# Kernel optimization log

Hardware: AMD Instinct MI355X
Metric: run time of the kernel (lower is better)

Reference implementation:

```python
import jax, jax.numpy as jnp
import numpy as np

B, T, D = 2, 1024, 768
H, HS = 12, 64          # n_head, head_size = n_embed // n_head
E, K = 8, 1             # num_experts, top-k (MoeLayer default k=1)
DF = 4 * D              # FFN hidden
EPS = 1e-5


def _ln(x, g, b):
    mu = jnp.mean(x, axis=-1, keepdims=True)
    var = jnp.mean(jnp.square(x - mu), axis=-1, keepdims=True)
    return (x - mu) * jax.lax.rsqrt(var + EPS) * g + b


def setup_inputs() -> dict:
    key = jax.random.key(0)
    ks = jax.random.split(key, 12)
    s = 0.02
    return {
        "x": jax.random.normal(ks[0], (B, T, D), dtype=jnp.float32),
        "ln1_g": jnp.ones((D,), jnp.float32),
        "ln1_b": jnp.zeros((D,), jnp.float32),
        "ln2_g": jnp.ones((D,), jnp.float32),
        "ln2_b": jnp.zeros((D,), jnp.float32),
        "Wq": jax.random.normal(ks[1], (H, D, HS), jnp.float32) * s,
        "Wk": jax.random.normal(ks[2], (H, D, HS), jnp.float32) * s,
        "Wv": jax.random.normal(ks[3], (H, D, HS), jnp.float32) * s,
        "Wp": jax.random.normal(ks[4], (D, D), jnp.float32) * s,
        "bp": jnp.zeros((D,), jnp.float32),
        "Wg": jax.random.normal(ks[5], (D, E), jnp.float32) * s,
        "W1": jax.random.normal(ks[6], (E, D, DF), jnp.float32) * s,
        "b1": jnp.zeros((E, DF), jnp.float32),
        "W2": jax.random.normal(ks[7], (E, DF, D), jnp.float32) * s,
        "b2": jnp.zeros((E, D), jnp.float32),
    }


def reference(x, ln1_g, ln1_b, ln2_g, ln2_b, Wq, Wk, Wv, Wp, bp, Wg, W1, b1, W2, b2):
    b, t, d = x.shape

    # ---- multi-head causal self-attention (per-head QKV, as in Head) ----
    h = _ln(x, ln1_g, ln1_b)
    q = jnp.einsum('btd,hds->bhts', h, Wq)
    k = jnp.einsum('btd,hds->bhts', h, Wk)
    v = jnp.einsum('btd,hds->bhts', h, Wv)
    # NOTE: original scales by C**-0.5 with C = n_embed (not head_size)
    scores = jnp.einsum('bhts,bhus->bhtu', q, k) * (d ** -0.5)
    causal = jnp.tril(jnp.ones((t, t), dtype=bool))
    scores = jnp.where(causal, scores, -jnp.inf)
    att = jax.nn.softmax(scores, axis=-1)
    out = jnp.einsum('bhtu,bhus->bhts', att, v)          # [B,H,T,HS]
    out = out.transpose(0, 2, 1, 3).reshape(b, t, d)     # concat heads
    x = x + out @ Wp + bp

    # ---- top-k MoE feed-forward (MoeLayer, k=1) ----
    h2 = _ln(x, ln2_g, ln2_b).reshape(-1, d)             # [N,D]
    gate_logits = h2 @ Wg                                # [N,E]
    w, sel = jax.lax.top_k(gate_logits, K)               # [N,K]
    w = jax.nn.softmax(w.astype(jnp.float32), axis=-1).astype(x.dtype)
    n = h2.shape[0]
    combine = jnp.zeros((n, Wg.shape[1]), x.dtype).at[
        jnp.arange(n)[:, None], sel].add(w)              # [N,E]
    hid = jax.nn.relu(jnp.einsum('nd,edf->enf', h2, W1) + b1[:, None, :])
    y = jnp.einsum('enf,efd->end', hid, W2) + b2[:, None, :]
    moe = jnp.einsum('ne,end->nd', combine, y)           # dense dispatch
    return x + moe.reshape(b, t, d)
```

## Files before the change

kernel.cpp:

```cpp
#include <hip/hip_runtime.h>
#include <math.h>

typedef __bf16 bf16;
typedef __bf16 bf16x8 __attribute__((ext_vector_type(8)));
typedef float f32x4 __attribute__((ext_vector_type(4)));

#define N_TOK 2048
#define DMODEL 768
#define NHEAD 12
#define TSEQ 1024
#define NEXP 8
#define DFF 3072

__device__ inline f32x4 mfma16(bf16x8 a, bf16x8 b, f32x4 c) {
    return __builtin_amdgcn_mfma_f32_16x16x32_bf16(a, b, c, 0, 0, 0);
}

__device__ inline f32x4 zero4() { f32x4 z = {0.f, 0.f, 0.f, 0.f}; return z; }

__device__ inline float block_sum(float v, float* red, int tid) {
#pragma unroll
    for (int off = 32; off > 0; off >>= 1) v += __shfl_down(v, off, 64);
    __syncthreads();
    if ((tid & 63) == 0) red[tid >> 6] = v;
    __syncthreads();
    return red[0] + red[1] + red[2] + red[3];
}

__global__ __launch_bounds__(256) void ln1_kernel(const float* __restrict__ x,
        const float* __restrict__ g, const float* __restrict__ b,
        bf16* __restrict__ hh, bf16* __restrict__ hl) {
    __shared__ float red[4];
    int row = blockIdx.x, tid = threadIdx.x;
    const float* xr = x + (size_t)row * DMODEL;
    float v[3];
#pragma unroll
    for (int i = 0; i < 3; i++) v[i] = xr[tid + i * 256];
    float s = block_sum(v[0] + v[1] + v[2], red, tid);
    float mu = s * (1.f / DMODEL);
    float q = 0.f;
#pragma unroll
    for (int i = 0; i < 3; i++) { float d = v[i] - mu; q += d * d; }
    q = block_sum(q, red, tid);
    float rstd = 1.0f / sqrtf(q * (1.f / DMODEL) + 1e-5f);
#pragma unroll
    for (int i = 0; i < 3; i++) {
        int d = tid + i * 256;
        float val = (v[i] - mu) * rstd * g[d] + b[d];
        bf16 hi = (bf16)val;
        hh[(size_t)row * DMODEL + d] = hi;
        hl[(size_t)row * DMODEL + d] = (bf16)(val - (float)hi);
    }
}

__device__ inline void gemm_step3(const bf16* lah, const bf16* lal,
                                  const bf16* lbh, const bf16* lbl,
                                  int wm, int wn, int row16, int quad,
                                  f32x4 acc[4][4]) {
    bf16x8 ah[4], al[4], bh[4], bl[4];
#pragma unroll
    for (int i = 0; i < 4; i++) {
        int ro = (wm * 64 + i * 16 + row16) * 40 + quad * 8;
        ah[i] = *(const bf16x8*)&lah[ro];
        al[i] = *(const bf16x8*)&lal[ro];
    }
#pragma unroll
    for (int i = 0; i < 4; i++) {
        int ro = (wn * 64 + i * 16 + row16) * 40 + quad * 8;
        bh[i] = *(const bf16x8*)&lbh[ro];
        bl[i] = *(const bf16x8*)&lbl[ro];
    }
#pragma unroll
    for (int mi = 0; mi < 4; mi++)
#pragma unroll
        for (int ni = 0; ni < 4; ni++) {
            acc[mi][ni] = mfma16(ah[mi], bh[ni], acc[mi][ni]);
            acc[mi][ni] = mfma16(ah[mi], bl[ni], acc[mi][ni]);
            acc[mi][ni] = mfma16(al[mi], bh[ni], acc[mi][ni]);
        }
}

__device__ inline void gemm_step1(const bf16* la, const bf16* lb, int wm, int wn,
                                  int row16, int quad, f32x4 acc[4][4]) {
    bf16x8 af[4], bfr[4];
#pragma unroll
    for (int i = 0; i < 4; i++)
        af[i] = *(const bf16x8*)&la[(wm * 64 + i * 16 + row16) * 40 + quad * 8];
#pragma unroll
    for (int i = 0; i < 4; i++)
        bfr[i] = *(const bf16x8*)&lb[(wn * 64 + i * 16 + row16) * 40 + quad * 8];
#pragma unroll
    for (int mi = 0; mi < 4; mi++)
#pragma unroll
        for (int ni = 0; ni < 4; ni++)
            acc[mi][ni] = mfma16(af[mi], bfr[ni], acc[mi][ni]);
}

#define TILE_E (128 * 40)

__global__ __launch_bounds__(256) void qkv_gemm(const bf16* __restrict__ hA_h,
        const bf16* __restrict__ hA_l,
        const float* __restrict__ Wq, const float* __restrict__ Wk,
        const float* __restrict__ Wv,
        bf16* __restrict__ qh, bf16* __restrict__ ql,
        bf16* __restrict__ kh, bf16* __restrict__ kl,
        bf16* __restrict__ vh, bf16* __restrict__ vl) {
    __shared__ alignas(16) bf16 lah[2 * TILE_E];
    __shared__ alignas(16) bf16 lal[2 * TILE_E];
    __shared__ alignas(16) bf16 lbh[2 * TILE_E];
    __shared__ alignas(16) bf16 lbl[2 * TILE_E];
    int tid = threadIdx.x;
    int m0 = blockIdx.y * 128;
    int nt = blockIdx.x;
    int sel = nt / 6;
    int n0 = (nt % 6) * 128;
    const float* W = (sel == 0) ? Wq : (sel == 1) ? Wk : Wv;
    bf16* obh = (sel == 0) ? qh : (sel == 1) ? kh : vh;
    bf16* obl = (sel == 0) ? ql : (sel == 1) ? kl : vl;
    int lane = tid & 63, w = tid >> 6, row16 = lane & 15, quad = lane >> 4;
    int wm = w >> 1, wn = w & 1;
    int r_a = tid >> 2, c_a = (tid & 3) << 3;
    int nW = tid & 127, kbase = tid >> 7;
    size_t wcol = (size_t)((n0 + nW) >> 6) * DMODEL * 64 + ((n0 + nW) & 63);
    f32x4 acc[4][4];
#pragma unroll
    for (int mi = 0; mi < 4; mi++)
#pragma unroll
        for (int ni = 0; ni < 4; ni++) acc[mi][ni] = zero4();
    const bf16* Ah = hA_h + (size_t)m0 * DMODEL;
    const bf16* Al = hA_l + (size_t)m0 * DMODEL;

    bf16x8 rAh0, rAh1, rAl0, rAl1;
    float wv[16];
    rAh0 = *(const bf16x8*)&Ah[(size_t)r_a * DMODEL + c_a];
    rAh1 = *(const bf16x8*)&Ah[(size_t)(r_a + 64) * DMODEL + c_a];
    rAl0 = *(const bf16x8*)&Al[(size_t)r_a * DMODEL + c_a];
    rAl1 = *(const bf16x8*)&Al[(size_t)(r_a + 64) * DMODEL + c_a];
#pragma unroll
    for (int i = 0; i < 16; i++) wv[i] = W[wcol + (size_t)(kbase + 2 * i) * 64];
    *(bf16x8*)&lah[r_a * 40 + c_a] = rAh0;
    *(bf16x8*)&lah[(r_a + 64) * 40 + c_a] = rAh1;
    *(bf16x8*)&lal[r_a * 40 + c_a] = rAl0;
    *(bf16x8*)&lal[(r_a + 64) * 40 + c_a] = rAl1;
#pragma unroll
    for (int i = 0; i < 16; i++) {
        bf16 hi = (bf16)wv[i];
        lbh[nW * 40 + kbase + 2 * i] = hi;
        lbl[nW * 40 + kbase + 2 * i] = (bf16)(wv[i] - (float)hi);
    }
    const int nk = DMODEL / 32;
    for (int ki = 0; ki < nk; ki++) {
        __syncthreads();
        int cur = (ki & 1) * TILE_E, nxt = ((ki + 1) & 1) * TILE_E;
        if (ki + 1 < nk) {
            int k0 = (ki + 1) * 32;
            rAh0 = *(const bf16x8*)&Ah[(size_t)r_a * DMODEL + k0 + c_a];
            rAh1 = *(const bf16x8*)&Ah[(size_t)(r_a + 64) * DMODEL + k0 + c_a];
            rAl0 = *(const bf16x8*)&Al[(size_t)r_a * DMODEL + k0 + c_a];
            rAl1 = *(const bf16x8*)&Al[(size_t)(r_a + 64) * DMODEL + k0 + c_a];
#pragma unroll
            for (int i = 0; i < 16; i++)
                wv[i] = W[wcol + (size_t)(k0 + kbase + 2 * i) * 64];
        }
        gemm_step3(lah + cur, lal + cur, lbh + cur, lbl + cur, wm, wn, row16, quad, acc);
        if (ki + 1 < nk) {
            *(bf16x8*)&lah[nxt + r_a * 40 + c_a] = rAh0;
            *(bf16x8*)&lah[nxt + (r_a + 64) * 40 + c_a] = rAh1;
            *(bf16x8*)&lal[nxt + r_a * 40 + c_a] = rAl0;
            *(bf16x8*)&lal[nxt + (r_a + 64) * 40 + c_a] = rAl1;
#pragma unroll
            for (int i = 0; i < 16; i++) {
                bf16 hi = (bf16)wv[i];
                lbh[nxt + nW * 40 + kbase + 2 * i] = hi;
                lbl[nxt + nW * 40 + kbase + 2 * i] = (bf16)(wv[i] - (float)hi);
            }
        }
    }
#pragma unroll
    for (int mi = 0; mi < 4; mi++) {
        int rowl = wm * 64 + mi * 16 + quad * 4;
#pragma unroll
        for (int ni = 0; ni < 4; ni++) {
            int col = n0 + wn * 64 + ni * 16 + row16;
            int hhd = col >> 6, s = col & 63;
#pragma unroll
            for (int r = 0; r < 4; r++) {
                int gm = m0 + rowl + r;
                int bb = gm >> 10, t = gm & 1023;
                size_t oi = (((size_t)bb * NHEAD + hhd) * TSEQ + t) * 64 + s;
                float val = acc[mi][ni][r];
                bf16 hi = (bf16)val;
                obh[oi] = hi;
                obl[oi] = (bf16)(val - (float)hi);
            }
        }
    }
}

__global__ __launch_bounds__(256) void attn_kernel(const bf16* __restrict__ qhb,
        const bf16* __restrict__ qlb, const bf16* __restrict__ khb,
        const bf16* __restrict__ klb, const bf16* __restrict__ vhb,
        const bf16* __restrict__ vlb, bf16* __restrict__ aoh,
        bf16* __restrict__ aol) {
    __shared__ alignas(16) bf16 kt_h[64 * 72];
    __shared__ alignas(16) bf16 kt_l[64 * 72];
    __shared__ alignas(16) bf16 vt_h[64 * 72];
    __shared__ alignas(16) bf16 vt_l[64 * 72];
    __shared__ alignas(16) bf16 p_h[4][16 * 72];
    __shared__ alignas(16) bf16 p_l[4][16 * 72];
    int qt = blockIdx.x, bh = blockIdx.y;
    int b = bh / NHEAD, hh = bh % NHEAD;
    int tid = threadIdx.x, lane = tid & 63, w = tid >> 6;
    int row16 = lane & 15, quad = lane >> 4;
    const bf16* qph = qhb + (size_t)bh * TSEQ * 64;
    const bf16* qpl = qlb + (size_t)bh * TSEQ * 64;
    const bf16* kph = khb + (size_t)bh * TSEQ * 64;
    const bf16* kpl = klb + (size_t)bh * TSEQ * 64;
    const bf16* vph = vhb + (size_t)bh * TSEQ * 64;
    const bf16* vpl = vlb + (size_t)bh * TSEQ * 64;
    int qrow = qt * 64 + w * 16 + row16;
    bf16x8 aq_h[2], aq_l[2];
#pragma unroll
    for (int kk = 0; kk < 2; kk++) {
        aq_h[kk] = *(const bf16x8*)&qph[(size_t)qrow * 64 + kk * 32 + quad * 8];
        aq_l[kk] = *(const bf16x8*)&qpl[(size_t)qrow * 64 + kk * 32 + quad * 8];
    }
    f32x4 o[4];
    float m_i[4], l_i[4];
#pragma unroll
    for (int i = 0; i < 4; i++) { o[i] = zero4(); m_i[i] = -INFINITY; l_i[i] = 0.f; }
    const float sc = 0.03608439182435161f;
    for (int kt = 0; kt <= qt; kt++) {
        __syncthreads();
#pragma unroll
        for (int i = 0; i < 2; i++) {
            int chunk = tid + i * 256;
            int r = chunk >> 3, c = (chunk & 7) << 3;
            size_t gi = (size_t)(kt * 64 + r) * 64 + c;
            *(bf16x8*)&kt_h[r * 72 + c] = *(const bf16x8*)&kph[gi];
            *(bf16x8*)&kt_l[r * 72 + c] = *(const bf16x8*)&kpl[gi];
        }
#pragma unroll
        for (int i = 0; i < 16; i++) {
            int idx = tid + (i << 8);
            int tk = idx >> 6, s = idx & 63;
            size_t gi = (size_t)(kt * 64 + tk) * 64 + s;
            vt_h[s * 72 + tk] = vph[gi];
            vt_l[s * 72 + tk] = vpl[gi];
        }
        __syncthreads();
        f32x4 sacc[4];
#pragma unroll
        for (int ni = 0; ni < 4; ni++) {
            sacc[ni] = zero4();
#pragma unroll
            for (int kk = 0; kk < 2; kk++) {
                int ro = (ni * 16 + row16) * 72 + kk * 32 + quad * 8;
                bf16x8 bk_h = *(const bf16x8*)&kt_h[ro];
                bf16x8 bk_l = *(const bf16x8*)&kt_l[ro];
                sacc[ni] = mfma16(aq_h[kk], bk_h, sacc[ni]);
                sacc[ni] = mfma16(aq_h[kk], bk_l, sacc[ni]);
                sacc[ni] = mfma16(aq_l[kk], bk_h, sacc[ni]);
            }
        }
        float mrow[4];
#pragma unroll
        for (int r = 0; r < 4; r++) mrow[r] = -INFINITY;
        int tq_b = qt * 64 + w * 16 + quad * 4;
#pragma unroll
        for (int ni = 0; ni < 4; ni++) {
            int tkg = kt * 64 + ni * 16 + row16;
#pragma unroll
            for (int r = 0; r < 4; r++) {
                float sv = sacc[ni][r] * sc;
                if (tkg > tq_b + r) sv = -INFINITY;
                sacc[ni][r] = sv;
                mrow[r] = fmaxf(mrow[r], sv);
            }
        }
#pragma unroll
        for (int r = 0; r < 4; r++) {
#pragma unroll
            for (int off = 8; off > 0; off >>= 1)
                mrow[r] = fmaxf(mrow[r], __shfl_xor(mrow[r], off, 16));
        }
        float alpha[4], rsum[4];
#pragma unroll
        for (int r = 0; r < 4; r++) {
            float nm = fmaxf(m_i[r], mrow[r]);
            alpha[r] = __expf(m_i[r] - nm);
            m_i[r] = nm;
            rsum[r] = 0.f;
        }
#pragma unroll
        for (int ni = 0; ni < 4; ni++)
#pragma unroll
            for (int r = 0; r < 4; r++) {
                float p = __expf(sacc[ni][r] - m_i[r]);
                sacc[ni][r] = p;
                rsum[r] += p;
            }
#pragma unroll
        for (int r = 0; r < 4; r++) {
#pragma unroll
            for (int off = 8; off > 0; off >>= 1)
                rsum[r] += __shfl_xor(rsum[r], off, 16);
            l_i[r] = l_i[r] * alpha[r] + rsum[r];
        }
#pragma unroll
        for (int ni = 0; ni < 4; ni++)
#pragma unroll
            for (int r = 0; r < 4; r++) o[ni][r] *= alpha[r];
#pragma unroll
        for (int ni = 0; ni < 4; ni++)
#pragma unroll
            for (int r = 0; r < 4; r++) {
                float p = sacc[ni][r];
                bf16 hi = (bf16)p;
                int po = (quad * 4 + r) * 72 + ni * 16 + row16;
                p_h[w][po] = hi;
                p_l[w][po] = (bf16)(p - (float)hi);
            }
        __syncthreads();
        bf16x8 ap_h[2], ap_l[2];
#pragma unroll
        for (int kk = 0; kk < 2; kk++) {
            ap_h[kk] = *(const bf16x8*)&p_h[w][row16 * 72 + kk * 32 + quad * 8];
            ap_l[kk] = *(const bf16x8*)&p_l[w][row16 * 72 + kk * 32 + quad * 8];
        }
#pragma unroll
        for (int ni = 0; ni < 4; ni++)
#pragma unroll
            for (int kk = 0; kk < 2; kk++) {
                int ro = (ni * 16 + row16) * 72 + kk * 32 + quad * 8;
                bf16x8 bv_h = *(const bf16x8*)&vt_h[ro];
                bf16x8 bv_l = *(const bf16x8*)&vt_l[ro];
                o[ni] = mfma16(ap_h[kk], bv_h, o[ni]);
                o[ni] = mfma16(ap_h[kk], bv_l, o[ni]);
                o[ni] = mfma16(ap_l[kk], bv_h, o[ni]);
            }
    }
    int t = qt * 64 + w * 16 + quad * 4;
#pragma unroll
    for (int ni = 0; ni < 4; ni++) {
        int col = hh * 64 + ni * 16 + row16;
#pragma unroll
        for (int r = 0; r < 4; r++) {
            float val = o[ni][r] / l_i[r];
            size_t n = (size_t)b * TSEQ + t + r;
            bf16 hi = (bf16)val;
            aoh[n * DMODEL + col] = hi;
            aol[n * DMODEL + col] = (bf16)(val - (float)hi);
        }
    }
}

__global__ __launch_bounds__(256) void proj_gemm(const bf16* __restrict__ aInH,
        const bf16* __restrict__ aInL,
        const float* __restrict__ Wp, const float* __restrict__ bp,
        const float* __restrict__ x, float* __restrict__ x1) {
    __shared__ alignas(16) bf16 lah[2 * TILE_E];
    __shared__ alignas(16) bf16 lal[2 * TILE_E];
    __shared__ alignas(16) bf16 lbh[2 * TILE_E];
    __shared__ alignas(16) bf16 lbl[2 * TILE_E];
    int tid = threadIdx.x;
    int m0 = blockIdx.y * 128, n0 = blockIdx.x * 128;
    int lane = tid & 63, w = tid >> 6, row16 = lane & 15, quad = lane >> 4;
    int wm = w >> 1, wn = w & 1;
    int r_a = tid >> 2, c_a = (tid & 3) << 3;
    int nW = tid & 127, kbase = tid >> 7;
    f32x4 acc[4][4];
#pragma unroll
    for (int mi = 0; mi < 4; mi++)
#pragma unroll
        for (int ni = 0; ni < 4; ni++) acc[mi][ni] = zero4();
    const bf16* Ah = aInH + (size_t)m0 * DMODEL;
    const bf16* Al = aInL + (size_t)m0 * DMODEL;
    bf16x8 rAh0, rAh1, rAl0, rAl1;
    float wv[16];
    rAh0 = *(const bf16x8*)&Ah[(size_t)r_a * DMODEL + c_a];
    rAh1 = *(const bf16x8*)&Ah[(size_t)(r_a + 64) * DMODEL + c_a];
    rAl0 = *(const bf16x8*)&Al[(size_t)r_a * DMODEL + c_a];
    rAl1 = *(const bf16x8*)&Al[(size_t)(r_a + 64) * DMODEL + c_a];
#pragma unroll
    for (int i = 0; i < 16; i++)
        wv[i] = Wp[(size_t)(kbase + 2 * i) * DMODEL + n0 + nW];
    *(bf16x8*)&lah[r_a * 40 + c_a] = rAh0;
    *(bf16x8*)&lah[(r_a + 64) * 40 + c_a] = rAh1;
    *(bf16x8*)&lal[r_a * 40 + c_a] = rAl0;
    *(bf16x8*)&lal[(r_a + 64) * 40 + c_a] = rAl1;
#pragma unroll
    for (int i = 0; i < 16; i++) {
        bf16 hi = (bf16)wv[i];
        lbh[nW * 40 + kbase + 2 * i] = hi;
        lbl[nW * 40 + kbase + 2 * i] = (bf16)(wv[i] - (float)hi);
    }
    const int nk = DMODEL / 32;
    for (int ki = 0; ki < nk; ki++) {
        __syncthreads();
        int cur = (ki & 1) * TILE_E, nxt = ((ki + 1) & 1) * TILE_E;
        if (ki + 1 < nk) {
            int k0 = (ki + 1) * 32;
            rAh0 = *(const bf16x8*)&Ah[(size_t)r_a * DMODEL + k0 + c_a];
            rAh1 = *(const bf16x8*)&Ah[(size_t)(r_a + 64) * DMODEL + k0 + c_a];
            rAl0 = *(const bf16x8*)&Al[(size_t)r_a * DMODEL + k0 + c_a];
            rAl1 = *(const bf16x8*)&Al[(size_t)(r_a + 64) * DMODEL + k0 + c_a];
#pragma unroll
            for (int i = 0; i < 16; i++)
                wv[i] = Wp[(size_t)(k0 + kbase + 2 * i) * DMODEL + n0 + nW];
        }
        gemm_step3(lah + cur, lal + cur, lbh + cur, lbl + cur, wm, wn, row16, quad, acc);
        if (ki + 1 < nk) {
            *(bf16x8*)&lah[nxt + r_a * 40 + c_a] = rAh0;
            *(bf16x8*)&lah[nxt + (r_a + 64) * 40 + c_a] = rAh1;
            *(bf16x8*)&lal[nxt + r_a * 40 + c_a] = rAl0;
            *(bf16x8*)&lal[nxt + (r_a + 64) * 40 + c_a] = rAl1;
#pragma unroll
            for (int i = 0; i < 16; i++) {
                bf16 hi = (bf16)wv[i];
                lbh[nxt + nW * 40 + kbase + 2 * i] = hi;
                lbl[nxt + nW * 40 + kbase + 2 * i] = (bf16)(wv[i] - (float)hi);
            }
        }
    }
#pragma unroll
    for (int mi = 0; mi < 4; mi++) {
        int rowl = wm * 64 + mi * 16 + quad * 4;
#pragma unroll
        for (int ni = 0; ni < 4; ni++) {
            int col = n0 + wn * 64 + ni * 16 + row16;
#pragma unroll
            for (int r = 0; r < 4; r++) {
                int gm = m0 + rowl + r;
                x1[(size_t)gm * DMODEL + col] =
                    acc[mi][ni][r] + bp[col] + x[(size_t)gm * DMODEL + col];
            }
        }
    }
}

__global__ __launch_bounds__(256) void ln2_gate_kernel(const float* __restrict__ x1,
        const float* __restrict__ g, const float* __restrict__ b,
        const float* __restrict__ Wg, bf16* __restrict__ h2,
        int* __restrict__ sel, int* __restrict__ counts) {
    __shared__ float red[4];
    __shared__ float glog[8];
    int row = blockIdx.x, tid = threadIdx.x;
    if (tid < 8) glog[tid] = 0.f;
    const float* xr = x1 + (size_t)row * DMODEL;
    float v[3];
#pragma unroll
    for (int i = 0; i < 3; i++) v[i] = xr[tid + i * 256];
    float s = block_sum(v[0] + v[1] + v[2], red, tid);
    float mu = s * (1.f / DMODEL);
    float qv = 0.f;
#pragma unroll
    for (int i = 0; i < 3; i++) { float d = v[i] - mu; qv += d * d; }
    qv = block_sum(qv, red, tid);
    float rstd = 1.0f / sqrtf(qv * (1.f / DMODEL) + 1e-5f);
    float ga[8];
#pragma unroll
    for (int e = 0; e < 8; e++) ga[e] = 0.f;
#pragma unroll
    for (int i = 0; i < 3; i++) {
        int d = tid + i * 256;
        float hv = (v[i] - mu) * rstd * g[d] + b[d];
        h2[(size_t)row * DMODEL + d] = (bf16)hv;
        const float* wgr = Wg + (size_t)d * NEXP;
#pragma unroll
        for (int e = 0; e < 8; e++) ga[e] += hv * wgr[e];
    }
#pragma unroll
    for (int e = 0; e < 8; e++)
#pragma unroll
        for (int off = 32; off > 0; off >>= 1) ga[e] += __shfl_down(ga[e], off, 64);
    if ((tid & 63) == 0)
#pragma unroll
        for (int e = 0; e < 8; e++) atomicAdd(&glog[e], ga[e]);
    __syncthreads();
    if (tid == 0) {
        float best = glog[0];
        int bi = 0;
#pragma unroll
        for (int e = 1; e < 8; e++)
            if (glog[e] > best) { best = glog[e]; bi = e; }
        sel[row] = bi;
        atomicAdd(&counts[bi], 1);
    }
}

__global__ void zero_kernel(int* __restrict__ p, int n) {
    int i = blockIdx.x * blockDim.x + threadIdx.x;
    if (i < n) p[i] = 0;
}
__global__ void zero_out_kernel(float* __restrict__ p) {
    int i = blockIdx.x * blockDim.x + threadIdx.x;
    f32x4 z = zero4();
    *(f32x4*)&p[i * 4] = z;
}
__global__ void scan_kernel(const int* __restrict__ counts, int* __restrict__ offsets) {
    if (threadIdx.x == 0) {
        int o = 0;
        for (int e = 0; e < NEXP; e++) { offsets[e] = o; o += counts[e]; }
    }
}
__global__ void scatter_kernel(const int* __restrict__ sel, const int* __restrict__ offsets,
                               int* __restrict__ cursor, int* __restrict__ perm) {
    int n = blockIdx.x * blockDim.x + threadIdx.x;
    if (n >= N_TOK) return;
    int e = sel[n];
    int pos = atomicAdd(&cursor[e], 1);
    perm[offsets[e] + pos] = n;
}

__global__ __launch_bounds__(256) void moe1_gemm(const bf16* __restrict__ h2,
        const float* __restrict__ W1, const float* __restrict__ b1,
        const int* __restrict__ counts, const int* __restrict__ offsets,
        const int* __restrict__ perm, bf16* __restrict__ hid) {
    int e = blockIdx.z;
    int cnt = counts[e];
    int rt = blockIdx.y;
    if (rt * 128 >= cnt) return;
    int off = offsets[e];
    int n0 = blockIdx.x * 128;
    const float* W = W1 + (size_t)e * DMODEL * DFF;
    __shared__ alignas(16) bf16 la[2 * TILE_E];
    __shared__ alignas(16) bf16 lb[2 * TILE_E];
    int tid = threadIdx.x;
    int lane = tid & 63, w = tid >> 6, row16 = lane & 15, quad = lane >> 4;
    int wm = w >> 1, wn = w & 1;
    int r_a = tid >> 2, c_a = (tid & 3) << 3;
    int nW = tid & 127, kbase = tid >> 7;
    int tok0 = perm[off + min(rt * 128 + r_a, cnt - 1)];
    int tok1 = perm[off + min(rt * 128 + r_a + 64, cnt - 1)];
    const bf16* a0 = h2 + (size_t)tok0 * DMODEL;
    const bf16* a1 = h2 + (size_t)tok1 * DMODEL;
    f32x4 acc[4][4];
#pragma unroll
    for (int mi = 0; mi < 4; mi++)
#pragma unroll
        for (int ni = 0; ni < 4; ni++) acc[mi][ni] = zero4();
    bf16x8 rA0, rA1;
    float wv[16];
    rA0 = *(const bf16x8*)&a0[c_a];
    rA1 = *(const bf16x8*)&a1[c_a];
#pragma unroll
    for (int i = 0; i < 16; i++)
        wv[i] = W[(size_t)(kbase + 2 * i) * DFF + n0 + nW];
    *(bf16x8*)&la[r_a * 40 + c_a] = rA0;
    *(bf16x8*)&la[(r_a + 64) * 40 + c_a] = rA1;
#pragma unroll
    for (int i = 0; i < 16; i++) lb[nW * 40 + kbase + 2 * i] = (bf16)wv[i];
    const int nk = DMODEL / 32;
    for (int ki = 0; ki < nk; ki++) {
        __syncthreads();
        int cur = (ki & 1) * TILE_E, nxt = ((ki + 1) & 1) * TILE_E;
        if (ki + 1 < nk) {
            int k0 = (ki + 1) * 32;
            rA0 = *(const bf16x8*)&a0[k0 + c_a];
            rA1 = *(const bf16x8*)&a1[k0 + c_a];
#pragma unroll
            for (int i = 0; i < 16; i++)
                wv[i] = W[(size_t)(k0 + kbase + 2 * i) * DFF + n0 + nW];
        }
        gemm_step1(la + cur, lb + cur, wm, wn, row16, quad, acc);
        if (ki + 1 < nk) {
            *(bf16x8*)&la[nxt + r_a * 40 + c_a] = rA0;
            *(bf16x8*)&la[nxt + (r_a + 64) * 40 + c_a] = rA1;
#pragma unroll
            for (int i = 0; i < 16; i++) lb[nxt + nW * 40 + kbase + 2 * i] = (bf16)wv[i];
        }
    }
#pragma unroll
    for (int mi = 0; mi < 4; mi++) {
        int rowl = wm * 64 + mi * 16 + quad * 4;
#pragma unroll
        for (int ni = 0; ni < 4; ni++) {
            int col = n0 + wn * 64 + ni * 16 + row16;
#pragma unroll
            for (int r = 0; r < 4; r++) {
                int lr = rowl + r;
                if (rt * 128 + lr < cnt) {
                    float val = acc[mi][ni][r] + b1[(size_t)e * DFF + col];
                    val = fmaxf(val, 0.f);
                    hid[(size_t)(off + rt * 128 + lr) * DFF + col] = (bf16)val;
                }
            }
        }
    }
}

__global__ __launch_bounds__(256) void moe2_gemm(const bf16* __restrict__ hid,
        const float* __restrict__ W2, const float* __restrict__ b2,
        const int* __restrict__ counts, const int* __restrict__ offsets,
        const int* __restrict__ perm, const float* __restrict__ x1,
        float* __restrict__ out) {
    int ez = blockIdx.z;
    int e = ez >> 1, ks = ez & 1;
    int cnt = counts[e];
    int rt = blockIdx.y;
    if (rt * 128 >= cnt) return;
    int off = offsets[e];
    int n0 = blockIdx.x * 128;
    const float* W = W2 + (size_t)e * DFF * DMODEL;
    __shared__ alignas(16) bf16 la[2 * TILE_E];
    __shared__ alignas(16) bf16 lb[2 * TILE_E];
    int tid = threadIdx.x;
    int lane = tid & 63, w = tid >> 6, row16 = lane & 15, quad = lane >> 4;
    int wm = w >> 1, wn = w & 1;
    int r_a = tid >> 2, c_a = (tid & 3) << 3;
    int nW = tid & 127, kbase = tid >> 7;
    const bf16* a0 = hid + (size_t)min(off + rt * 128 + r_a, N_TOK - 1) * DFF;
    const bf16* a1 = hid + (size_t)min(off + rt * 128 + r_a + 64, N_TOK - 1) * DFF;
    f32x4 acc[4][4];
#pragma unroll
    for (int mi = 0; mi < 4; mi++)
#pragma unroll
        for (int ni = 0; ni < 4; ni++) acc[mi][ni] = zero4();
    const int kst = ks * (DFF / 2);
    bf16x8 rA0, rA1;
    float wv[16];
    rA0 = *(const bf16x8*)&a0[kst + c_a];
    rA1 = *(const bf16x8*)&a1[kst + c_a];
#pragma unroll
    for (int i = 0; i < 16; i++)
        wv[i] = W[(size_t)(kst + kbase + 2 * i) * DMODEL + n0 + nW];
    *(bf16x8*)&la[r_a * 40 + c_a] = rA0;
    *(bf16x8*)&la[(r_a + 64) * 40 + c_a] = rA1;
#pragma unroll
    for (int i = 0; i < 16; i++) lb[nW * 40 + kbase + 2 * i] = (bf16)wv[i];
    const int nk = (DFF / 2) / 32;
    for (int ki = 0; ki < nk; ki++) {
        __syncthreads();
        int cur = (ki & 1) * TILE_E, nxt = ((ki + 1) & 1) * TILE_E;
        if (ki + 1 < nk) {
            int k0 = kst + (ki + 1) * 32;
            rA0 = *(const bf16x8*)&a0[k0 + c_a];
            rA1 = *(const bf16x8*)&a1[k0 + c_a];
#pragma unroll
            for (int i = 0; i < 16; i++)
                wv[i] = W[(size_t)(k0 + kbase + 2 * i) * DMODEL + n0 + nW];
        }
        gemm_step1(la + cur, lb + cur, wm, wn, row16, quad, acc);
        if (ki + 1 < nk) {
            *(bf16x8*)&la[nxt + r_a * 40 + c_a] = rA0;
            *(bf16x8*)&la[nxt + (r_a + 64) * 40 + c_a] = rA1;
#pragma unroll
            for (int i = 0; i < 16; i++) lb[nxt + nW * 40 + kbase + 2 * i] = (bf16)wv[i];
        }
    }
#pragma unroll
    for (int mi = 0; mi < 4; mi++) {
        int rowl = wm * 64 + mi * 16 + quad * 4;
#pragma unroll
        for (int ni = 0; ni < 4; ni++) {
            int col = n0 + wn * 64 + ni * 16 + row16;
#pragma unroll
            for (int r = 0; r < 4; r++) {
                int lr = rowl + r;
                if (rt * 128 + lr < cnt) {
                    int n = perm[off + rt * 128 + lr];
                    float val = acc[mi][ni][r];
                    if (ks == 0)
                        val += b2[(size_t)e * DMODEL + col] + x1[(size_t)n * DMODEL + col];
                    atomicAdd(&out[(size_t)n * DMODEL + col], val);
                }
            }
        }
    }
}

extern "C" void kernel_launch(void* const* d_in, const int* in_sizes, int n_in,
                              void* d_out, int out_size, void* d_ws, size_t ws_size,
                              hipStream_t stream) {
    const float* x    = (const float*)d_in[0];
    const float* ln1g = (const float*)d_in[1];
    const float* ln1b = (const float*)d_in[2];
    const float* ln2g = (const float*)d_in[3];
    const float* ln2b = (const float*)d_in[4];
    const float* Wq   = (const float*)d_in[5];
    const float* Wk   = (const float*)d_in[6];
    const float* Wv   = (const float*)d_in[7];
    const float* Wp   = (const float*)d_in[8];
    const float* bp   = (const float*)d_in[9];
    const float* Wg   = (const float*)d_in[10];
    const float* W1   = (const float*)d_in[11];
    const float* b1   = (const float*)d_in[12];
    const float* W2   = (const float*)d_in[13];
    const float* b2   = (const float*)d_in[14];
    float* out = (float*)d_out;

    char* ws = (char*)d_ws;
    size_t off = 0;
    const size_t SZ = (size_t)N_TOK * DMODEL * 2;
    bf16* h1h = (bf16*)(ws + off); off += SZ;
    bf16* h1l = (bf16*)(ws + off); off += SZ;
    bf16* qh  = (bf16*)(ws + off); off += SZ;
    bf16* ql  = (bf16*)(ws + off); off += SZ;
    bf16* kh  = (bf16*)(ws + off); off += SZ;
    bf16* kl  = (bf16*)(ws + off); off += SZ;
    bf16* vh  = (bf16*)(ws + off); off += SZ;
    bf16* vl  = (bf16*)(ws + off); off += SZ;
    bf16* aoh = (bf16*)(ws + off); off += SZ;
    bf16* aol = (bf16*)(ws + off); off += SZ;
    float* x1 = (float*)(ws + off); off += (size_t)N_TOK * DMODEL * 4;
    bf16* h2  = (bf16*)(ws + off); off += SZ;
    bf16* hid = (bf16*)(ws + off); off += (size_t)N_TOK * DFF * 2;
    int* counts  = (int*)(ws + off); off += 8 * 4;
    int* cursor  = (int*)(ws + off); off += 8 * 4;
    int* offsets = (int*)(ws + off); off += 8 * 4;
    int* sel     = (int*)(ws + off); off += (size_t)N_TOK * 4;
    int* perm    = (int*)(ws + off); off += (size_t)N_TOK * 4;

    zero_kernel<<<1, 64, 0, stream>>>(counts, 16);
    zero_out_kernel<<<N_TOK * DMODEL / 4 / 256, 256, 0, stream>>>(out);
    ln1_kernel<<<N_TOK, 256, 0, stream>>>(x, ln1g, ln1b, h1h, h1l);
    qkv_gemm<<<dim3(18, 16), 256, 0, stream>>>(h1h, h1l, Wq, Wk, Wv, qh, ql, kh, kl, vh, vl);
    attn_kernel<<<dim3(16, 24), 256, 0, stream>>>(qh, ql, kh, kl, vh, vl, aoh, aol);
    proj_gemm<<<dim3(6, 16), 256, 0, stream>>>(aoh, aol, Wp, bp, x, x1);
    ln2_gate_kernel<<<N_TOK, 256, 0, stream>>>(x1, ln2g, ln2b, Wg, h2, sel, counts);
    scan_kernel<<<1, 64, 0, stream>>>(counts, offsets);
    scatter_kernel<<<8, 256, 0, stream>>>(sel, offsets, cursor, perm);
    moe1_gemm<<<dim3(24, 16, 8), 256, 0, stream>>>(h2, W1, b1, counts, offsets, perm, hid);
    moe2_gemm<<<dim3(6, 16, 16), 256, 0, stream>>>(hid, W2, b2, counts, offsets, perm, x1, out);
}
```

Measured before the change: 540.0 us.

## Fold zeroing and scan into other kernels, vectorize LDS weight stores, widen MoE2 split-K

Drops the zero, zero_out and scan launches. Zeroing of counts and the output moves into ln1_kernel, and each consumer recomputes expert offsets from counts. Weight staging now gives each thread 16 contiguous k values, so the converted bf16 values go to LDS as 4-wide vector stores instead of scalar strided ones. The V transpose in attention also packs 4 values per LDS store. MoE2 split-K goes from 2 to 4 slices to get more blocks, at the cost of more atomicAdds into the output.

```diff
diff --git a/kernel.cpp b/kernel.cpp
--- a/kernel.cpp
+++ b/kernel.cpp
@@ -2,6 +2,7 @@
 #include <math.h>
 
 typedef __bf16 bf16;
+typedef __bf16 bf16x4 __attribute__((ext_vector_type(4)));
 typedef __bf16 bf16x8 __attribute__((ext_vector_type(8)));
 typedef float f32x4 __attribute__((ext_vector_type(4)));
 
@@ -29,9 +30,13 @@
 
 __global__ __launch_bounds__(256) void ln1_kernel(const float* __restrict__ x,
         const float* __restrict__ g, const float* __restrict__ b,
-        bf16* __restrict__ hh, bf16* __restrict__ hl) {
+        bf16* __restrict__ hh, bf16* __restrict__ hl,
+        int* __restrict__ cz, float* __restrict__ outz) {
     __shared__ float red[4];
     int row = blockIdx.x, tid = threadIdx.x;
+    if (row == 0 && tid < 16) cz[tid] = 0;
+#pragma unroll
+    for (int i = 0; i < 3; i++) outz[(size_t)row * DMODEL + tid + i * 256] = 0.f;
     const float* xr = x + (size_t)row * DMODEL;
     float v[3];
 #pragma unroll
@@ -97,6 +102,31 @@
 }
 
 #define TILE_E (128 * 40)
+
+__device__ inline void wstore_hilo(bf16* lbh, bf16* lbl, int base, const float* wv) {
+#pragma unroll
+    for (int gq = 0; gq < 4; gq++) {
+        bf16x4 ph, pl;
+#pragma unroll
+        for (int j = 0; j < 4; j++) {
+            float v = wv[gq * 4 + j];
+            bf16 hi = (bf16)v;
+            ph[j] = hi;
+            pl[j] = (bf16)(v - (float)hi);
+        }
+        *(bf16x4*)&lbh[base + gq * 4] = ph;
+        *(bf16x4*)&lbl[base + gq * 4] = pl;
+    }
+}
+__device__ inline void wstore1(bf16* lb, int base, const float* wv) {
+#pragma unroll
+    for (int gq = 0; gq < 4; gq++) {
+        bf16x4 p;
+#pragma unroll
+        for (int j = 0; j < 4; j++) p[j] = (bf16)wv[gq * 4 + j];
+        *(bf16x4*)&lb[base + gq * 4] = p;
+    }
+}
 
 __global__ __launch_bounds__(256) void qkv_gemm(const bf16* __restrict__ hA_h,
         const bf16* __restrict__ hA_l,
@@ -120,8 +150,9 @@
     int lane = tid & 63, w = tid >> 6, row16 = lane & 15, quad = lane >> 4;
     int wm = w >> 1, wn = w & 1;
     int r_a = tid >> 2, c_a = (tid & 3) << 3;
-    int nW = tid & 127, kbase = tid >> 7;
+    int nW = tid & 127, kb16 = (tid >> 7) * 16;
     size_t wcol = (size_t)((n0 + nW) >> 6) * DMODEL * 64 + ((n0 + nW) & 63);
+    int wbase = nW * 40 + kb16;
     f32x4 acc[4][4];
 #pragma unroll
     for (int mi = 0; mi < 4; mi++)
@@ -129,7 +160,6 @@
         for (int ni = 0; ni < 4; ni++) acc[mi][ni] = zero4();
     const bf16* Ah = hA_h + (size_t)m0 * DMODEL;
     const bf16* Al = hA_l + (size_t)m0 * DMODEL;
-
     bf16x8 rAh0, rAh1, rAl0, rAl1;
     float wv[16];
     rAh0 = *(const bf16x8*)&Ah[(size_t)r_a * DMODEL + c_a];
@@ -137,17 +167,12 @@
     rAl0 = *(const bf16x8*)&Al[(size_t)r_a * DMODEL + c_a];
     rAl1 = *(const bf16x8*)&Al[(size_t)(r_a + 64) * DMODEL + c_a];
 #pragma unroll
-    for (int i = 0; i < 16; i++) wv[i] = W[wcol + (size_t)(kbase + 2 * i) * 64];
+    for (int i = 0; i < 16; i++) wv[i] = W[wcol + (size_t)(kb16 + i) * 64];
     *(bf16x8*)&lah[r_a * 40 + c_a] = rAh0;
     *(bf16x8*)&lah[(r_a + 64) * 40 + c_a] = rAh1;
     *(bf16x8*)&lal[r_a * 40 + c_a] = rAl0;
     *(bf16x8*)&lal[(r_a + 64) * 40 + c_a] = rAl1;
-#pragma unroll
-    for (int i = 0; i < 16; i++) {
-        bf16 hi = (bf16)wv[i];
-        lbh[nW * 40 + kbase + 2 * i] = hi;
-        lbl[nW * 40 + kbase + 2 * i] = (bf16)(wv[i] - (float)hi);
-    }
+    wstore_hilo(lbh, lbl, wbase, wv);
     const int nk = DMODEL / 32;
     for (int ki = 0; ki < nk; ki++) {
         __syncthreads();
@@ -160,7 +185,7 @@
             rAl1 = *(const bf16x8*)&Al[(size_t)(r_a + 64) * DMODEL + k0 + c_a];
 #pragma unroll
             for (int i = 0; i < 16; i++)
-                wv[i] = W[wcol + (size_t)(k0 + kbase + 2 * i) * 64];
+                wv[i] = W[wcol + (size_t)(k0 + kb16 + i) * 64];
         }
         gemm_step3(lah + cur, lal + cur, lbh + cur, lbl + cur, wm, wn, row16, quad, acc);
         if (ki + 1 < nk) {
@@ -168,12 +193,7 @@
             *(bf16x8*)&lah[nxt + (r_a + 64) * 40 + c_a] = rAh1;
             *(bf16x8*)&lal[nxt + r_a * 40 + c_a] = rAl0;
             *(bf16x8*)&lal[nxt + (r_a + 64) * 40 + c_a] = rAl1;
-#pragma unroll
-            for (int i = 0; i < 16; i++) {
-                bf16 hi = (bf16)wv[i];
-                lbh[nxt + nW * 40 + kbase + 2 * i] = hi;
-                lbl[nxt + nW * 40 + kbase + 2 * i] = (bf16)(wv[i] - (float)hi);
-            }
+            wstore_hilo(lbh + nxt, lbl + nxt, wbase, wv);
         }
     }
 #pragma unroll
@@ -241,12 +261,18 @@
             *(bf16x8*)&kt_l[r * 72 + c] = *(const bf16x8*)&kpl[gi];
         }
 #pragma unroll
-        for (int i = 0; i < 16; i++) {
-            int idx = tid + (i << 8);
-            int tk = idx >> 6, s = idx & 63;
-            size_t gi = (size_t)(kt * 64 + tk) * 64 + s;
-            vt_h[s * 72 + tk] = vph[gi];
-            vt_l[s * 72 + tk] = vpl[gi];
+        for (int u = 0; u < 4; u++) {
+            int unit = tid + u * 256;
+            int s = unit & 63, tg = unit >> 6;
+            bf16x4 ph, pl;
+#pragma unroll
+            for (int j = 0; j < 4; j++) {
+                size_t gi = (size_t)(kt * 64 + tg * 4 + j) * 64 + s;
+                ph[j] = vph[gi];
+                pl[j] = vpl[gi];
+            }
+            *(bf16x4*)&vt_h[s * 72 + tg * 4] = ph;
+            *(bf16x4*)&vt_l[s * 72 + tg * 4] = pl;
         }
         __syncthreads();
         f32x4 sacc[4];
@@ -368,7 +394,8 @@
     int lane = tid & 63, w = tid >> 6, row16 = lane & 15, quad = lane >> 4;
     int wm = w >> 1, wn = w & 1;
     int r_a = tid >> 2, c_a = (tid & 3) << 3;
-    int nW = tid & 127, kbase = tid >> 7;
+    int nW = tid & 127, kb16 = (tid >> 7) * 16;
+    int wbase = nW * 40 + kb16;
     f32x4 acc[4][4];
 #pragma unroll
     for (int mi = 0; mi < 4; mi++)
@@ -384,17 +411,12 @@
     rAl1 = *(const bf16x8*)&Al[(size_t)(r_a + 64) * DMODEL + c_a];
 #pragma unroll
     for (int i = 0; i < 16; i++)
-        wv[i] = Wp[(size_t)(kbase + 2 * i) * DMODEL + n0 + nW];
+        wv[i] = Wp[(size_t)(kb16 + i) * DMODEL + n0 + nW];
     *(bf16x8*)&lah[r_a * 40 + c_a] = rAh0;
     *(bf16x8*)&lah[(r_a + 64) * 40 + c_a] = rAh1;
     *(bf16x8*)&lal[r_a * 40 + c_a] = rAl0;
     *(bf16x8*)&lal[(r_a + 64) * 40 + c_a] = rAl1;
-#pragma unroll
-    for (int i = 0; i < 16; i++) {
-        bf16 hi = (bf16)wv[i];
-        lbh[nW * 40 + kbase + 2 * i] = hi;
-        lbl[nW * 40 + kbase + 2 * i] = (bf16)(wv[i] - (float)hi);
-    }
+    wstore_hilo(lbh, lbl, wbase, wv);
     const int nk = DMODEL / 32;
     for (int ki = 0; ki < nk; ki++) {
         __syncthreads();
@@ -407,7 +429,7 @@
             rAl1 = *(const bf16x8*)&Al[(size_t)(r_a + 64) * DMODEL + k0 + c_a];
 #pragma unroll
             for (int i = 0; i < 16; i++)
-                wv[i] = Wp[(size_t)(k0 + kbase + 2 * i) * DMODEL + n0 + nW];
+                wv[i] = Wp[(size_t)(k0 + kb16 + i) * DMODEL + n0 + nW];
         }
         gemm_step3(lah + cur, lal + cur, lbh + cur, lbl + cur, wm, wn, row16, quad, acc);
         if (ki + 1 < nk) {
@@ -415,12 +437,7 @@
             *(bf16x8*)&lah[nxt + (r_a + 64) * 40 + c_a] = rAh1;
             *(bf16x8*)&lal[nxt + r_a * 40 + c_a] = rAl0;
             *(bf16x8*)&lal[nxt + (r_a + 64) * 40 + c_a] = rAl1;
-#pragma unroll
-            for (int i = 0; i < 16; i++) {
-                bf16 hi = (bf16)wv[i];
-                lbh[nxt + nW * 40 + kbase + 2 * i] = hi;
-                lbl[nxt + nW * 40 + kbase + 2 * i] = (bf16)(wv[i] - (float)hi);
-            }
+            wstore_hilo(lbh + nxt, lbl + nxt, wbase, wv);
         }
     }
 #pragma unroll
@@ -489,39 +506,27 @@
     }
 }
 
-__global__ void zero_kernel(int* __restrict__ p, int n) {
-    int i = blockIdx.x * blockDim.x + threadIdx.x;
-    if (i < n) p[i] = 0;
-}
-__global__ void zero_out_kernel(float* __restrict__ p) {
-    int i = blockIdx.x * blockDim.x + threadIdx.x;
-    f32x4 z = zero4();
-    *(f32x4*)&p[i * 4] = z;
-}
-__global__ void scan_kernel(const int* __restrict__ counts, int* __restrict__ offsets) {
-    if (threadIdx.x == 0) {
-        int o = 0;
-        for (int e = 0; e < NEXP; e++) { offsets[e] = o; o += counts[e]; }
-    }
-}
-__global__ void scatter_kernel(const int* __restrict__ sel, const int* __restrict__ offsets,
+__global__ void scatter_kernel(const int* __restrict__ sel, const int* __restrict__ counts,
                                int* __restrict__ cursor, int* __restrict__ perm) {
     int n = blockIdx.x * blockDim.x + threadIdx.x;
     if (n >= N_TOK) return;
     int e = sel[n];
+    int off = 0;
+    for (int i = 0; i < NEXP; i++) off += (i < e) ? counts[i] : 0;
     int pos = atomicAdd(&cursor[e], 1);
-    perm[offsets[e] + pos] = n;
+    perm[off + pos] = n;
 }
 
 __global__ __launch_bounds__(256) void moe1_gemm(const bf16* __restrict__ h2,
         const float* __restrict__ W1, const float* __restrict__ b1,
-        const int* __restrict__ counts, const int* __restrict__ offsets,
-        const int* __restrict__ perm, bf16* __restrict__ hid) {
+        const int* __restrict__ counts, const int* __restrict__ perm,
+        bf16* __restrict__ hid) {
     int e = blockIdx.z;
     int cnt = counts[e];
     int rt = blockIdx.y;
     if (rt * 128 >= cnt) return;
-    int off = offsets[e];
+    int off = 0;
+    for (int i = 0; i < NEXP; i++) off += (i < e) ? counts[i] : 0;
     int n0 = blockIdx.x * 128;
     const float* W = W1 + (size_t)e * DMODEL * DFF;
     __shared__ alignas(16) bf16 la[2 * TILE_E];
@@ -530,7 +535,8 @@
     int lane = tid & 63, w = tid >> 6, row16 = lane & 15, quad = lane >> 4;
     int wm = w >> 1, wn = w & 1;
     int r_a = tid >> 2, c_a = (tid & 3) << 3;
-    int nW = tid & 127, kbase = tid >> 7;
+    int nW = tid & 127, kb16 = (tid >> 7) * 16;
+    int wbase = nW * 40 + kb16;
     int tok0 = perm[off + min(rt * 128 + r_a, cnt - 1)];
     int tok1 = perm[off + min(rt * 128 + r_a + 64, cnt - 1)];
     const bf16* a0 = h2 + (size_t)tok0 * DMODEL;
@@ -546,11 +552,10 @@
     rA1 = *(const bf16x8*)&a1[c_a];
 #pragma unroll
     for (int i = 0; i < 16; i++)
-        wv[i] = W[(size_t)(kbase + 2 * i) * DFF + n0 + nW];
+        wv[i] = W[(size_t)(kb16 + i) * DFF + n0 + nW];
     *(bf16x8*)&la[r_a * 40 + c_a] = rA0;
     *(bf16x8*)&la[(r_a + 64) * 40 + c_a] = rA1;
-#pragma unroll
-    for (int i = 0; i < 16; i++) lb[nW * 40 + kbase + 2 * i] = (bf16)wv[i];
+    wstore1(lb, wbase, wv);
     const int nk = DMODEL / 32;
     for (int ki = 0; ki < nk; ki++) {
         __syncthreads();
@@ -561,14 +566,13 @@
             rA1 = *(const bf16x8*)&a1[k0 + c_a];
 #pragma unroll
             for (int i = 0; i < 16; i++)
-                wv[i] = W[(size_t)(k0 + kbase + 2 * i) * DFF + n0 + nW];
+                wv[i] = W[(size_t)(k0 + kb16 + i) * DFF + n0 + nW];
         }
         gemm_step1(la + cur, lb + cur, wm, wn, row16, quad, acc);
         if (ki + 1 < nk) {
             *(bf16x8*)&la[nxt + r_a * 40 + c_a] = rA0;
             *(bf16x8*)&la[nxt + (r_a + 64) * 40 + c_a] = rA1;
-#pragma unroll
-            for (int i = 0; i < 16; i++) lb[nxt + nW * 40 + kbase + 2 * i] = (bf16)wv[i];
+            wstore1(lb + nxt, wbase, wv);
         }
     }
 #pragma unroll
@@ -592,15 +596,15 @@
 
 __global__ __launch_bounds__(256) void moe2_gemm(const bf16* __restrict__ hid,
         const float* __restrict__ W2, const float* __restrict__ b2,
-        const int* __restrict__ counts, const int* __restrict__ offsets,
-        const int* __restrict__ perm, const float* __restrict__ x1,
-        float* __restrict__ out) {
+        const int* __restrict__ counts, const int* __restrict__ perm,
+        const float* __restrict__ x1, float* __restrict__ out) {
     int ez = blockIdx.z;
-    int e = ez >> 1, ks = ez & 1;
+    int e = ez & 7, ks = ez >> 3;
     int cnt = counts[e];
     int rt = blockIdx.y;
     if (rt * 128 >= cnt) return;
-    int off = offsets[e];
+    int off = 0;
+    for (int i = 0; i < NEXP; i++) off += (i < e) ? counts[i] : 0;
     int n0 = blockIdx.x * 128;
     const float* W = W2 + (size_t)e * DFF * DMODEL;
     __shared__ alignas(16) bf16 la[2 * TILE_E];
@@ -609,7 +613,8 @@
     int lane = tid & 63, w = tid >> 6, row16 = lane & 15, quad = lane >> 4;
     int wm = w >> 1, wn = w & 1;
     int r_a = tid >> 2, c_a = (tid & 3) << 3;
-    int nW = tid & 127, kbase = tid >> 7;
+    int nW = tid & 127, kb16 = (tid >> 7) * 16;
+    int wbase = nW * 40 + kb16;
     const bf16* a0 = hid + (size_t)min(off + rt * 128 + r_a, N_TOK - 1) * DFF;
     const bf16* a1 = hid + (size_t)min(off + rt * 128 + r_a + 64, N_TOK - 1) * DFF;
     f32x4 acc[4][4];
@@ -617,19 +622,18 @@
     for (int mi = 0; mi < 4; mi++)
 #pragma unroll
         for (int ni = 0; ni < 4; ni++) acc[mi][ni] = zero4();
-    const int kst = ks * (DFF / 2);
+    const int kst = ks * (DFF / 4);
     bf16x8 rA0, rA1;
     float wv[16];
     rA0 = *(const bf16x8*)&a0[kst + c_a];
     rA1 = *(const bf16x8*)&a1[kst + c_a];
 #pragma unroll
     for (int i = 0; i < 16; i++)
-        wv[i] = W[(size_t)(kst + kbase + 2 * i) * DMODEL + n0 + nW];
+        wv[i] = W[(size_t)(kst + kb16 + i) * DMODEL + n0 + nW];
     *(bf16x8*)&la[r_a * 40 + c_a] = rA0;
     *(bf16x8*)&la[(r_a + 64) * 40 + c_a] = rA1;
-#pragma unroll
-    for (int i = 0; i < 16; i++) lb[nW * 40 + kbase + 2 * i] = (bf16)wv[i];
-    const int nk = (DFF / 2) / 32;
+    wstore1(lb, wbase, wv);
+    const int nk = (DFF / 4) / 32;
     for (int ki = 0; ki < nk; ki++) {
         __syncthreads();
         int cur = (ki & 1) * TILE_E, nxt = ((ki + 1) & 1) * TILE_E;
@@ -639,14 +643,13 @@
             rA1 = *(const bf16x8*)&a1[k0 + c_a];
 #pragma unroll
             for (int i = 0; i < 16; i++)
-                wv[i] = W[(size_t)(k0 + kbase + 2 * i) * DMODEL + n0 + nW];
+                wv[i] = W[(size_t)(k0 + kb16 + i) * DMODEL + n0 + nW];
         }
         gemm_step1(la + cur, lb + cur, wm, wn, row16, quad, acc);
         if (ki + 1 < nk) {
             *(bf16x8*)&la[nxt + r_a * 40 + c_a] = rA0;
             *(bf16x8*)&la[nxt + (r_a + 64) * 40 + c_a] = rA1;
-#pragma unroll
-            for (int i = 0; i < 16; i++) lb[nxt + nW * 40 + kbase + 2 * i] = (bf16)wv[i];
+            wstore1(lb + nxt, wbase, wv);
         }
     }
 #pragma unroll
@@ -708,19 +711,15 @@
     bf16* hid = (bf16*)(ws + off); off += (size_t)N_TOK * DFF * 2;
     int* counts  = (int*)(ws + off); off += 8 * 4;
     int* cursor  = (int*)(ws + off); off += 8 * 4;
-    int* offsets = (int*)(ws + off); off += 8 * 4;
     int* sel     = (int*)(ws + off); off += (size_t)N_TOK * 4;
     int* perm    = (int*)(ws + off); off += (size_t)N_TOK * 4;
 
-    zero_kernel<<<1, 64, 0, stream>>>(counts, 16);
-    zero_out_kernel<<<N_TOK * DMODEL / 4 / 256, 256, 0, stream>>>(out);
-    ln1_kernel<<<N_TOK, 256, 0, stream>>>(x, ln1g, ln1b, h1h, h1l);
+    ln1_kernel<<<N_TOK, 256, 0, stream>>>(x, ln1g, ln1b, h1h, h1l, counts, out);
     qkv_gemm<<<dim3(18, 16), 256, 0, stream>>>(h1h, h1l, Wq, Wk, Wv, qh, ql, kh, kl, vh, vl);
     attn_kernel<<<dim3(16, 24), 256, 0, stream>>>(qh, ql, kh, kl, vh, vl, aoh, aol);
     proj_gemm<<<dim3(6, 16), 256, 0, stream>>>(aoh, aol, Wp, bp, x, x1);
     ln2_gate_kernel<<<N_TOK, 256, 0, stream>>>(x1, ln2g, ln2b, Wg, h2, sel, counts);
-    scan_kernel<<<1, 64, 0, stream>>>(counts, offsets);
-    scatter_kernel<<<8, 256, 0, stream>>>(sel, offsets, cursor, perm);
-    moe1_gemm<<<dim3(24, 16, 8), 256, 0, stream>>>(h2, W1, b1, counts, offsets, perm, hid);
-    moe2_gemm<<<dim3(6, 16, 16), 256, 0, stream>>>(hid, W2, b2, counts, offsets, perm, x1, out);
-}
+    scatter_kernel<<<8, 256, 0, stream>>>(sel, counts, cursor, perm);
+    moe1_gemm<<<dim3(24, 16, 8), 256, 0, stream>>>(h2, W1, b1, counts, perm, hid);
+    moe2_gemm<<<dim3(6, 16, 32), 256, 0, stream>>>(hid, W2, b2, counts, perm, x1, out);
+}
```

Result: faster. 511.8 us (-5.2%).
